# Kernel optimization log

Hardware: AMD Instinct MI355X
Metric: run time of the kernel (lower is better)

The kernel has to match this reference:

```python
import jax, jax.numpy as jnp
import numpy as np
import math

N_BITS = 3
N_EMBD = 2048
N_HEAD = 16
B, T = 1, 2048


def fake_quant_act(x, bits=N_BITS):
    # Brevitas Int8ActPerTensorFloat at 3 bits: signed, non-narrow range [-4, 3]
    qmin, qmax = -(2 ** (bits - 1)), 2 ** (bits - 1) - 1
    s = jax.lax.stop_gradient(jnp.max(jnp.abs(x))) / (2 ** (bits - 1))
    q = jnp.clip(jnp.round(x / s), qmin, qmax) * s
    return x + jax.lax.stop_gradient(q - x)  # STE


def fake_quant_weight(w, bits=N_BITS):
    # Int8WeightPerTensorFloat, narrow_range=True at 3 bits: range [-3, 3]
    qmax = 2 ** (bits - 1) - 1
    s = jax.lax.stop_gradient(jnp.max(jnp.abs(w))) / qmax
    q = jnp.clip(jnp.round(w / s), -qmax, qmax) * s
    return w + jax.lax.stop_gradient(q - w)  # STE


def setup_inputs() -> dict:
    key = jax.random.key(0)
    ks = jax.random.split(key, 7)
    W_STD = 0.02  # GPT-style init keeps exp(att) in range (own_softmax has no max-subtract)
    x = jax.random.normal(ks[0], (B, T, N_EMBD), dtype=jnp.float32)
    W1 = jax.random.normal(ks[1], (N_EMBD, N_EMBD), dtype=jnp.float32) * W_STD
    W2 = jax.random.normal(ks[2], (N_EMBD, N_EMBD), dtype=jnp.float32) * W_STD
    W3 = jax.random.normal(ks[3], (N_EMBD, N_EMBD), dtype=jnp.float32) * W_STD
    b1 = jax.random.normal(ks[4], (N_EMBD,), dtype=jnp.float32) * W_STD
    b2 = jax.random.normal(ks[5], (N_EMBD,), dtype=jnp.float32) * W_STD
    b3 = jax.random.normal(ks[6], (N_EMBD,), dtype=jnp.float32) * W_STD
    return {"x": x, "W1": W1, "b1": b1, "W2": W2, "b2": b2, "W3": W3, "b3": b3}


def reference(x, W1, b1, W2, b2, W3, b3):
    hs = N_EMBD // N_HEAD
    xq = fake_quant_act(x)  # quant_inp
    q = xq @ fake_quant_weight(W1).T + b1  # c_attn1
    k = xq @ fake_quant_weight(W2).T + b2  # c_attn2
    v = xq @ fake_quant_weight(W3).T + b3  # c_attn3
    # [B,T,C] -> [B,nh,T,hs]
    q = q.reshape(B, T, N_HEAD, hs).transpose(0, 2, 1, 3)
    k = k.reshape(B, T, N_HEAD, hs).transpose(0, 2, 1, 3)
    v = v.reshape(B, T, N_HEAD, hs).transpose(0, 2, 1, 3)
    att = jnp.einsum("bhqd,bhkd->bhqk", q, k) * (1.0 / math.sqrt(hs))
    # own_softmax: exp normalized over dim=1 == the HEAD axis (faithful to source; no mask)
    e = jnp.exp(att)
    att = e / jnp.sum(e, axis=1, keepdims=True)
    # attn_dropout p=0 -> identity; c_proj never applied in forward
    y = jnp.einsum("bhqk,bhkd->bhqd", att, v)  # [B,nh,T,hs]
    return y
```

## Files before the change

### kernel.cpp

```cpp
#include <hip/hip_runtime.h>
#include <hip/hip_bf16.h>

typedef short bf16x8 __attribute__((ext_vector_type(8)));
typedef float f32x4 __attribute__((ext_vector_type(4)));
typedef unsigned short u16;

constexpr int TOKS = 2048;
constexpr int EMB  = 2048;
constexpr int NH   = 16;
constexpr int HS   = 128;
constexpr float RSQ = 0.08838834764831845f;

constexpr size_t OFF_SCAL = 0;
constexpr size_t OFF_QX   = 1024;
constexpr size_t SZ_MAT   = (size_t)TOKS * EMB * 2;
constexpr size_t OFF_QW   = OFF_QX + SZ_MAT;
constexpr size_t OFF_Q    = OFF_QW + 3 * SZ_MAT;
constexpr size_t OFF_K    = OFF_Q + SZ_MAT;
constexpr size_t OFF_V    = OFF_K + SZ_MAT;
constexpr size_t OFF_VT   = OFF_V + SZ_MAT;
constexpr size_t OFF_DEN  = OFF_VT + SZ_MAT;

#define VMCNT(n) asm volatile("s_waitcnt vmcnt(" #n ")" ::: "memory")
#define LGKM0()  asm volatile("s_waitcnt lgkmcnt(0)" ::: "memory")
#define BAR()    do { asm volatile("" ::: "memory"); __builtin_amdgcn_s_barrier(); asm volatile("" ::: "memory"); } while (0)

__device__ __forceinline__ u16 f2b(float f) {
  unsigned u = __float_as_uint(f);
  unsigned r = (u + 0x7fffu + ((u >> 16) & 1u)) >> 16;
  return (u16)r;
}

__device__ __forceinline__ unsigned cvtpk(float a, float b) {
  unsigned r;
  asm("v_cvt_pk_bf16_f32 %0, %1, %2" : "=v"(r) : "v"(a), "v"(b));
  return r;
}

__device__ __forceinline__ void gload16(const void* g, void* l) {
  __builtin_amdgcn_global_load_lds(
      (const __attribute__((address_space(1))) unsigned int*)g,
      (__attribute__((address_space(3))) unsigned int*)l, 16, 0, 0);
}

__global__ void k_init(int* scal) {
  if (threadIdx.x < 4) scal[threadIdx.x] = 0;
}

__global__ void k_absmax(const float* __restrict__ x, const float* __restrict__ w1,
                         const float* __restrict__ w2, const float* __restrict__ w3,
                         int* scal) {
  const float* src = (blockIdx.y == 0) ? x : (blockIdx.y == 1) ? w1 : (blockIdx.y == 2) ? w2 : w3;
  const float4* s4 = (const float4*)src;
  int idx = blockIdx.x * 256 + threadIdx.x;
  float m = 0.f;
  for (int i = 0; i < 16; ++i) {
    float4 v = s4[idx + i * 65536];
    m = fmaxf(m, fmaxf(fmaxf(fabsf(v.x), fabsf(v.y)), fmaxf(fabsf(v.z), fabsf(v.w))));
  }
  for (int o = 32; o; o >>= 1) m = fmaxf(m, __shfl_down(m, o));
  __shared__ float red[4];
  if ((threadIdx.x & 63) == 0) red[threadIdx.x >> 6] = m;
  __syncthreads();
  if (threadIdx.x == 0) {
    m = fmaxf(fmaxf(red[0], red[1]), fmaxf(red[2], red[3]));
    atomicMax(&scal[blockIdx.y], __float_as_int(m));
  }
}

__global__ void k_quant(const float* __restrict__ x, const float* __restrict__ w1,
                        const float* __restrict__ w2, const float* __restrict__ w3,
                        u16* qx, u16* qw, const int* scal) {
  int a = blockIdx.y;
  const float* src = (a == 0) ? x : (a == 1) ? w1 : (a == 2) ? w2 : w3;
  u16* dst = (a == 0) ? qx : qw + (size_t)(a - 1) * TOKS * EMB;
  float mx = __int_as_float(scal[a]);
  float s = (a == 0) ? mx * 0.25f : mx / 3.0f;
  float lo = (a == 0) ? -4.f : -3.f;
  const float hi = 3.f;
  int idx = blockIdx.x * 256 + threadIdx.x;
  for (int i = 0; i < 16; ++i) {
    int j = idx + i * 65536;
    float4 v = ((const float4*)src)[j];
    ushort4 o;
    o.x = f2b(fminf(fmaxf(rintf(v.x / s), lo), hi));
    o.y = f2b(fminf(fmaxf(rintf(v.y / s), lo), hi));
    o.z = f2b(fminf(fmaxf(rintf(v.z / s), lo), hi));
    o.w = f2b(fminf(fmaxf(rintf(v.w / s), lo), hi));
    ((ushort4*)dst)[j] = o;
  }
}

__global__ __launch_bounds__(256, 3) void k_gemm(const u16* __restrict__ qx, const u16* __restrict__ qw,
    const float* __restrict__ b1, const float* __restrict__ b2, const float* __restrict__ b3,
    const int* __restrict__ scal, u16* qo, u16* ko, u16* vo) {
  int z = blockIdx.z;
  const u16* W = qw + (size_t)z * TOKS * EMB;
  const float* bias = (z == 0) ? b1 : (z == 1) ? b2 : b3;
  u16* out = (z == 0) ? qo : (z == 1) ? ko : vo;
  float sx = __int_as_float(scal[0]) * 0.25f;
  float sw = __int_as_float(scal[1 + z]) / 3.0f;
  float alpha = sx * sw;
  float extra = (z == 0) ? RSQ : 1.0f;
  int t0 = blockIdx.y * 128, o0 = blockIdx.x * 128;
  __shared__ __align__(16) u16 As[128 * 64];
  __shared__ __align__(16) u16 Bs[128 * 64];
  int tid = threadIdx.x, lane = tid & 63, wid = tid >> 6;
  int mh = (wid >> 1) * 64, nh = (wid & 1) * 64;
  f32x4 acc[4][4] = {};
  const char* Ab = (const char*)qx;
  const char* Bb = (const char*)W;
  for (int kk = 0; kk < 32; ++kk) {
#pragma unroll
    for (int p = 0; p < 4; ++p) {
      int L = p * 4096 + tid * 16;
      int r = L >> 7;
      int s = ((L >> 4) & 7) ^ (r & 7);
      gload16(Ab + (size_t)(t0 + r) * 4096 + kk * 128 + s * 16,
              (char*)As + p * 4096 + wid * 1024);
      gload16(Bb + (size_t)(o0 + r) * 4096 + kk * 128 + s * 16,
              (char*)Bs + p * 4096 + wid * 1024);
    }
    __syncthreads();
#pragma unroll
    for (int ks = 0; ks < 2; ++ks) {
      bf16x8 af[4], bfr[4];
#pragma unroll
      for (int m = 0; m < 4; ++m) {
        int row = mh + m * 16 + (lane & 15);
        int sl = (ks * 4 + (lane >> 4)) ^ (row & 7);
        af[m] = *(const bf16x8*)((const char*)As + row * 128 + sl * 16);
      }
#pragma unroll
      for (int n = 0; n < 4; ++n) {
        int row = nh + n * 16 + (lane & 15);
        int sl = (ks * 4 + (lane >> 4)) ^ (row & 7);
        bfr[n] = *(const bf16x8*)((const char*)Bs + row * 128 + sl * 16);
      }
#pragma unroll
      for (int m = 0; m < 4; ++m)
#pragma unroll
        for (int n = 0; n < 4; ++n)
          acc[m][n] = __builtin_amdgcn_mfma_f32_16x16x32_bf16(af[m], bfr[n], acc[m][n], 0, 0, 0);
    }
    __syncthreads();
  }
#pragma unroll
  for (int m = 0; m < 4; ++m)
#pragma unroll
    for (int n = 0; n < 4; ++n) {
      int ocol = o0 + nh + n * 16 + (lane & 15);
      float bb = bias[ocol];
#pragma unroll
      for (int r = 0; r < 4; ++r) {
        int trow = t0 + mh + m * 16 + (lane >> 4) * 4 + r;
        float v = (acc[m][n][r] * alpha + bb) * extra;
        out[(size_t)trow * EMB + ocol] = f2b(v);
      }
    }
}

__global__ void k_transpose(const u16* __restrict__ v, u16* vt) {
  int h = blockIdx.z, d0 = blockIdx.y * 64, t0 = blockIdx.x * 64;
  __shared__ u16 tile[64][65];
  int tid = threadIdx.x;
  for (int i = 0; i < 16; ++i) {
    int idx = i * 256 + tid, r = idx >> 6, c = idx & 63;
    tile[r][c] = v[(size_t)(t0 + r) * EMB + h * HS + d0 + c];
  }
  __syncthreads();
  for (int i = 0; i < 16; ++i) {
    int idx = i * 256 + tid, r = idx >> 6, c = idx & 63;
    vt[(size_t)(h * HS + d0 + r) * TOKS + t0 + c] = tile[c][r];
  }
}

__global__ __launch_bounds__(256, 3) void k_denom(const u16* __restrict__ q, const u16* __restrict__ k,
                                                  float* __restrict__ invden) {
  int bid = blockIdx.x;
  int qy = bid & 15, kx = bid >> 4;
  int qt0 = qy * 128, kt0 = kx * 64;
  __shared__ __align__(16) u16 Qs[2][128 * 64];
  __shared__ __align__(16) u16 Ksm[2][64 * 64];
  int tid = threadIdx.x, lane = tid & 63, wid = tid >> 6;
  int wq = (wid >> 1) * 64, wk = (wid & 1) * 32;
  f32x4 acc[4][2] = {}, dd[4][2] = {};
  auto stage = [&](int st, int buf) {
#pragma unroll
    for (int p = 0; p < 4; ++p) {
      int L = p * 4096 + tid * 16;
      int r = L >> 7;
      int s = ((L >> 4) & 7) ^ (r & 7);
      gload16((const char*)q + (size_t)(qt0 + r) * 4096 + st * 128 + s * 16,
              (char*)Qs[buf] + p * 4096 + wid * 1024);
    }
#pragma unroll
    for (int p = 0; p < 2; ++p) {
      int L = p * 4096 + tid * 16;
      int r = L >> 7;
      int s = ((L >> 4) & 7) ^ (r & 7);
      gload16((const char*)k + (size_t)(kt0 + r) * 4096 + st * 128 + s * 16,
              (char*)Ksm[buf] + p * 4096 + wid * 1024);
    }
  };
  stage(0, 0);
  for (int st = 0; st < 32; ++st) {
    int cur = st & 1;
    if (st < 31) { stage(st + 1, cur ^ 1); VMCNT(6); } else { VMCNT(0); }
    BAR();
    __builtin_amdgcn_s_setprio(1);
#pragma unroll
    for (int ks = 0; ks < 2; ++ks) {
      bf16x8 af[4], bfr[2];
#pragma unroll
      for (int m = 0; m < 4; ++m) {
        int row = wq + m * 16 + (lane & 15);
        int sl = (ks * 4 + (lane >> 4)) ^ (row & 7);
        af[m] = *(const bf16x8*)((const char*)Qs[cur] + row * 128 + sl * 16);
      }
#pragma unroll
      for (int n = 0; n < 2; ++n) {
        int row = wk + n * 16 + (lane & 15);
        int sl = (ks * 4 + (lane >> 4)) ^ (row & 7);
        bfr[n] = *(const bf16x8*)((const char*)Ksm[cur] + row * 128 + sl * 16);
      }
#pragma unroll
      for (int m = 0; m < 4; ++m)
#pragma unroll
        for (int n = 0; n < 2; ++n)
          acc[m][n] = __builtin_amdgcn_mfma_f32_16x16x32_bf16(af[m], bfr[n], acc[m][n], 0, 0, 0);
    }
    __builtin_amdgcn_s_setprio(0);
    BAR();
    if (st & 1) {
#pragma unroll
      for (int m = 0; m < 4; ++m)
#pragma unroll
        for (int n = 0; n < 2; ++n) {
#pragma unroll
          for (int r = 0; r < 4; ++r) dd[m][n][r] += __expf(acc[m][n][r]);
          acc[m][n] = f32x4{0.f, 0.f, 0.f, 0.f};
        }
    }
  }
#pragma unroll
  for (int m = 0; m < 4; ++m)
#pragma unroll
    for (int n = 0; n < 2; ++n)
#pragma unroll
      for (int r = 0; r < 4; ++r) {
        int qrow = qt0 + wq + m * 16 + (lane >> 4) * 4 + r;
        int kcol = kt0 + wk + n * 16 + (lane & 15);
        invden[(size_t)qrow * TOKS + kcol] = 1.0f / dd[m][n][r];
      }
}

__global__ __launch_bounds__(256, 2) void k_attn(const u16* __restrict__ q, const u16* __restrict__ k,
                                                 const u16* __restrict__ vt, const float* __restrict__ invden,
                                                 float* __restrict__ out) {
  int bid = blockIdx.x;
  int h = bid & 15, qt0 = (bid >> 4) * 64;
  __shared__ __align__(16) u16 Ks[2][64 * 128];
  __shared__ __align__(16) u16 Vs[2][128 * 64];
  __shared__ __align__(16) u16 Ps[64 * 64];
  int tid = threadIdx.x, lane = tid & 63, wid = tid >> 6;

  auto stageKV = [&](int kb, int buf) {
#pragma unroll
    for (int p = 0; p < 4; ++p) {
      int L = p * 4096 + tid * 16;
      int r = L >> 8;
      int s = ((L >> 4) & 15) ^ (r & 7);
      gload16((const char*)k + (size_t)(kb * 64 + r) * 4096 + h * 256 + s * 16,
              (char*)Ks[buf] + p * 4096 + wid * 1024);
    }
#pragma unroll
    for (int p = 0; p < 4; ++p) {
      int L = p * 4096 + tid * 16;
      int r = L >> 7;
      int s = ((L >> 4) & 7) ^ (r & 7);
      gload16((const char*)vt + (size_t)(h * HS + r) * 4096 + kb * 128 + s * 16,
              (char*)Vs[buf] + p * 4096 + wid * 1024);
    }
  };
  stageKV(0, 0);
  bf16x8 qf[4][4];
#pragma unroll
  for (int m = 0; m < 4; ++m)
#pragma unroll
    for (int c = 0; c < 4; ++c)
      qf[m][c] = *(const bf16x8*)(q + (size_t)(qt0 + m * 16 + (lane & 15)) * EMB
                                  + h * HS + c * 32 + (lane >> 4) * 8);
  f32x4 yacc[4][2] = {};
  const float* dinv = invden + (size_t)qt0 * TOKS;
  for (int kb = 0; kb < 32; ++kb) {
    int cur = kb & 1;
    if (kb < 31) { stageKV(kb + 1, cur ^ 1); VMCNT(12); } else { VMCNT(4); }
    BAR();
    f32x4 pacc[4] = {};
    __builtin_amdgcn_s_setprio(1);
#pragma unroll
    for (int c = 0; c < 4; ++c) {
      int row = wid * 16 + (lane & 15);
      int sl = (c * 4 + (lane >> 4)) ^ (row & 7);
      bf16x8 bk = *(const bf16x8*)((const char*)Ks[cur] + row * 256 + sl * 16);
#pragma unroll
      for (int m = 0; m < 4; ++m)
        pacc[m] = __builtin_amdgcn_mfma_f32_16x16x32_bf16(bk, qf[m][c], pacc[m], 0, 0, 0);
    }
    __builtin_amdgcn_s_setprio(0);
#pragma unroll
    for (int m = 0; m < 4; ++m) {
      int qr = m * 16 + (lane & 15);
      float4 dv = *(const float4*)&dinv[(size_t)qr * TOKS + kb * 64 + wid * 16 + (lane >> 4) * 4];
      float e0 = __expf(pacc[m][0]) * dv.x;
      float e1 = __expf(pacc[m][1]) * dv.y;
      float e2 = __expf(pacc[m][2]) * dv.z;
      float e3 = __expf(pacc[m][3]) * dv.w;
      uint2 pk;
      pk.x = cvtpk(e0, e1);
      pk.y = cvtpk(e2, e3);
      int kby = wid * 32 + (lane >> 4) * 8;
      *(uint2*)((char*)Ps + qr * 128 + (kby ^ ((qr & 7) << 4))) = pk;
    }
    if (kb < 31) { VMCNT(8); } else { VMCNT(0); }
    LGKM0();
    BAR();
    __builtin_amdgcn_s_setprio(1);
#pragma unroll
    for (int ks = 0; ks < 2; ++ks) {
      bf16x8 pa[4], bv[2];
#pragma unroll
      for (int m = 0; m < 4; ++m) {
        int row = m * 16 + (lane & 15);
        int off = (ks * 64 + (lane >> 4) * 16) ^ ((row & 7) << 4);
        pa[m] = *(const bf16x8*)((const char*)Ps + row * 128 + off);
      }
#pragma unroll
      for (int j = 0; j < 2; ++j) {
        int row = wid * 32 + j * 16 + (lane & 15);
        int sl = (ks * 4 + (lane >> 4)) ^ (row & 7);
        bv[j] = *(const bf16x8*)((const char*)Vs[cur] + row * 128 + sl * 16);
      }
#pragma unroll
      for (int m = 0; m < 4; ++m)
#pragma unroll
        for (int j = 0; j < 2; ++j)
          yacc[m][j] = __builtin_amdgcn_mfma_f32_16x16x32_bf16(pa[m], bv[j], yacc[m][j], 0, 0, 0);
    }
    __builtin_amdgcn_s_setprio(0);
    BAR();
  }
#pragma unroll
  for (int m = 0; m < 4; ++m)
#pragma unroll
    for (int j = 0; j < 2; ++j)
#pragma unroll
      for (int r = 0; r < 4; ++r) {
        int trow = qt0 + m * 16 + (lane >> 4) * 4 + r;
        int dcol = wid * 32 + j * 16 + (lane & 15);
        out[(size_t)(h * TOKS + trow) * HS + dcol] = yacc[m][j][r];
      }
}

extern "C" void kernel_launch(void* const* d_in, const int* in_sizes, int n_in,
                              void* d_out, int out_size, void* d_ws, size_t ws_size,
                              hipStream_t stream) {
  const float* x  = (const float*)d_in[0];
  const float* W1 = (const float*)d_in[1];
  const float* b1 = (const float*)d_in[2];
  const float* W2 = (const float*)d_in[3];
  const float* b2 = (const float*)d_in[4];
  const float* W3 = (const float*)d_in[5];
  const float* b3 = (const float*)d_in[6];
  char* ws = (char*)d_ws;
  int*   scal   = (int*)(ws + OFF_SCAL);
  u16*   qx     = (u16*)(ws + OFF_QX);
  u16*   qw     = (u16*)(ws + OFF_QW);
  u16*   qo     = (u16*)(ws + OFF_Q);
  u16*   ko     = (u16*)(ws + OFF_K);
  u16*   vo     = (u16*)(ws + OFF_V);
  u16*   vt     = (u16*)(ws + OFF_VT);
  float* invden = (float*)(ws + OFF_DEN);
  float* y      = (float*)d_out;

  hipLaunchKernelGGL(k_init, dim3(1), dim3(64), 0, stream, scal);
  hipLaunchKernelGGL(k_absmax, dim3(256, 4), dim3(256), 0, stream, x, W1, W2, W3, scal);
  hipLaunchKernelGGL(k_quant, dim3(256, 4), dim3(256), 0, stream, x, W1, W2, W3, qx, qw, scal);
  hipLaunchKernelGGL(k_gemm, dim3(16, 16, 3), dim3(256), 0, stream,
                     qx, qw, b1, b2, b3, scal, qo, ko, vo);
  hipLaunchKernelGGL(k_transpose, dim3(32, 2, 16), dim3(256), 0, stream, vo, vt);
  hipLaunchKernelGGL(k_denom, dim3(512), dim3(256), 0, stream, qo, ko, invden);
  hipLaunchKernelGGL(k_attn, dim3(512), dim3(256), 0, stream, qo, ko, vt, invden, y);
}
```

Before: 207.5 us.

## Store inverse denominators as bf16 and prefetch them one block ahead

The inverse softmax denominators go from fp32 to bf16, which halves the 16 MB write in k_denom and the matching read in k_attn. k_attn now prefetches the next key block's denominators into registers alongside the K/V stage, ping-ponging between two register sets in a manually unrolled loop. This removes the blocking global load before the exp step. The head/block mapping is also permuted to change L2 locality. The cost is reduced precision of the denominators and higher register pressure.

```diff
diff --git a/kernel.cpp b/kernel.cpp
--- a/kernel.cpp
+++ b/kernel.cpp
@@ -176,7 +176,7 @@
 }
 
 __global__ __launch_bounds__(256, 3) void k_denom(const u16* __restrict__ q, const u16* __restrict__ k,
-                                                  float* __restrict__ invden) {
+                                                  u16* __restrict__ invden) {
   int bid = blockIdx.x;
   int qy = bid & 15, kx = bid >> 4;
   int qt0 = qy * 128, kt0 = kx * 64;
@@ -251,15 +251,16 @@
       for (int r = 0; r < 4; ++r) {
         int qrow = qt0 + wq + m * 16 + (lane >> 4) * 4 + r;
         int kcol = kt0 + wk + n * 16 + (lane & 15);
-        invden[(size_t)qrow * TOKS + kcol] = 1.0f / dd[m][n][r];
+        invden[(size_t)qrow * TOKS + kcol] = f2b(1.0f / dd[m][n][r]);
       }
 }
 
 __global__ __launch_bounds__(256, 2) void k_attn(const u16* __restrict__ q, const u16* __restrict__ k,
-                                                 const u16* __restrict__ vt, const float* __restrict__ invden,
+                                                 const u16* __restrict__ vt, const u16* __restrict__ invden,
                                                  float* __restrict__ out) {
   int bid = blockIdx.x;
-  int h = bid & 15, qt0 = (bid >> 4) * 64;
+  int h = (bid & 7) * 2 + ((bid >> 3) & 1);
+  int qt0 = (bid >> 4) * 64;
   __shared__ __align__(16) u16 Ks[2][64 * 128];
   __shared__ __align__(16) u16 Vs[2][128 * 64];
   __shared__ __align__(16) u16 Ps[64 * 64];
@@ -283,7 +284,15 @@
               (char*)Vs[buf] + p * 4096 + wid * 1024);
     }
   };
+  const u16* dinv = invden + (size_t)qt0 * TOKS;
+  uint2 dvA[4], dvB[4];
+
   stageKV(0, 0);
+#pragma unroll
+  for (int m = 0; m < 4; ++m) {
+    int qr = m * 16 + (lane & 15);
+    dvA[m] = *(const uint2*)&dinv[(size_t)qr * TOKS + wid * 16 + (lane >> 4) * 4];
+  }
   bf16x8 qf[4][4];
 #pragma unroll
   for (int m = 0; m < 4; ++m)
@@ -292,65 +301,88 @@
       qf[m][c] = *(const bf16x8*)(q + (size_t)(qt0 + m * 16 + (lane & 15)) * EMB
                                   + h * HS + c * 32 + (lane >> 4) * 8);
   f32x4 yacc[4][2] = {};
-  const float* dinv = invden + (size_t)qt0 * TOKS;
-  for (int kb = 0; kb < 32; ++kb) {
-    int cur = kb & 1;
-    if (kb < 31) { stageKV(kb + 1, cur ^ 1); VMCNT(12); } else { VMCNT(4); }
-    BAR();
-    f32x4 pacc[4] = {};
-    __builtin_amdgcn_s_setprio(1);
-#pragma unroll
-    for (int c = 0; c < 4; ++c) {
-      int row = wid * 16 + (lane & 15);
-      int sl = (c * 4 + (lane >> 4)) ^ (row & 7);
-      bf16x8 bk = *(const bf16x8*)((const char*)Ks[cur] + row * 256 + sl * 16);
-#pragma unroll
-      for (int m = 0; m < 4; ++m)
-        pacc[m] = __builtin_amdgcn_mfma_f32_16x16x32_bf16(bk, qf[m][c], pacc[m], 0, 0, 0);
-    }
-    __builtin_amdgcn_s_setprio(0);
-#pragma unroll
-    for (int m = 0; m < 4; ++m) {
-      int qr = m * 16 + (lane & 15);
-      float4 dv = *(const float4*)&dinv[(size_t)qr * TOKS + kb * 64 + wid * 16 + (lane >> 4) * 4];
-      float e0 = __expf(pacc[m][0]) * dv.x;
-      float e1 = __expf(pacc[m][1]) * dv.y;
-      float e2 = __expf(pacc[m][2]) * dv.z;
-      float e3 = __expf(pacc[m][3]) * dv.w;
-      uint2 pk;
-      pk.x = cvtpk(e0, e1);
-      pk.y = cvtpk(e2, e3);
-      int kby = wid * 32 + (lane >> 4) * 8;
-      *(uint2*)((char*)Ps + qr * 128 + (kby ^ ((qr & 7) << 4))) = pk;
-    }
-    if (kb < 31) { VMCNT(8); } else { VMCNT(0); }
-    LGKM0();
-    BAR();
-    __builtin_amdgcn_s_setprio(1);
-#pragma unroll
-    for (int ks = 0; ks < 2; ++ks) {
-      bf16x8 pa[4], bv[2];
-#pragma unroll
-      for (int m = 0; m < 4; ++m) {
-        int row = m * 16 + (lane & 15);
-        int off = (ks * 64 + (lane >> 4) * 16) ^ ((row & 7) << 4);
-        pa[m] = *(const bf16x8*)((const char*)Ps + row * 128 + off);
-      }
-#pragma unroll
-      for (int j = 0; j < 2; ++j) {
-        int row = wid * 32 + j * 16 + (lane & 15);
-        int sl = (ks * 4 + (lane >> 4)) ^ (row & 7);
-        bv[j] = *(const bf16x8*)((const char*)Vs[cur] + row * 128 + sl * 16);
-      }
-#pragma unroll
-      for (int m = 0; m < 4; ++m)
-#pragma unroll
-        for (int j = 0; j < 2; ++j)
-          yacc[m][j] = __builtin_amdgcn_mfma_f32_16x16x32_bf16(pa[m], bv[j], yacc[m][j], 0, 0, 0);
-    }
-    __builtin_amdgcn_s_setprio(0);
-    BAR();
-  }
+
+#define ITER(KB, CUR, DVU, DVP, LAST)                                           \
+  {                                                                             \
+    if (!(LAST)) {                                                              \
+      stageKV((KB) + 1, (CUR) ^ 1);                                             \
+      _Pragma("unroll")                                                         \
+      for (int m = 0; m < 4; ++m) {                                             \
+        int qr = m * 16 + (lane & 15);                                          \
+        DVP[m] = *(const uint2*)&dinv[(size_t)qr * TOKS + ((KB) + 1) * 64 +     \
+                                      wid * 16 + (lane >> 4) * 4];              \
+      }                                                                         \
+      VMCNT(12);                                                                \
+    } else {                                                                    \
+      VMCNT(0);                                                                 \
+    }                                                                           \
+    BAR();                                                                      \
+    f32x4 pacc[4] = {};                                                         \
+    __builtin_amdgcn_s_setprio(1);                                              \
+    _Pragma("unroll")                                                           \
+    for (int c = 0; c < 4; ++c) {                                               \
+      int row = wid * 16 + (lane & 15);                                         \
+      int sl = (c * 4 + (lane >> 4)) ^ (row & 7);                               \
+      bf16x8 bk = *(const bf16x8*)((const char*)Ks[CUR] + row * 256 + sl * 16); \
+      _Pragma("unroll")                                                         \
+      for (int m = 0; m < 4; ++m)                                               \
+        pacc[m] = __builtin_amdgcn_mfma_f32_16x16x32_bf16(bk, qf[m][c], pacc[m], 0, 0, 0); \
+    }                                                                           \
+    __builtin_amdgcn_s_setprio(0);                                              \
+    _Pragma("unroll")                                                           \
+    for (int m = 0; m < 4; ++m) {                                               \
+      int qr = m * 16 + (lane & 15);                                            \
+      float d0 = __uint_as_float(DVU[m].x << 16);                               \
+      float d1 = __uint_as_float(DVU[m].x & 0xffff0000u);                       \
+      float d2 = __uint_as_float(DVU[m].y << 16);                               \
+      float d3 = __uint_as_float(DVU[m].y & 0xffff0000u);                       \
+      float e0 = __expf(pacc[m][0]) * d0;                                       \
+      float e1 = __expf(pacc[m][1]) * d1;                                       \
+      float e2 = __expf(pacc[m][2]) * d2;                                       \
+      float e3 = __expf(pacc[m][3]) * d3;                                       \
+      uint2 pk;                                                                 \
+      pk.x = cvtpk(e0, e1);                                                     \
+      pk.y = cvtpk(e2, e3);                                                     \
+      int kby = wid * 32 + (lane >> 4) * 8;                                     \
+      *(uint2*)((char*)Ps + qr * 128 + (kby ^ ((qr & 7) << 4))) = pk;           \
+    }                                                                           \
+    LGKM0();                                                                    \
+    BAR();                                                                      \
+    __builtin_amdgcn_s_setprio(1);                                              \
+    _Pragma("unroll")                                                           \
+    for (int ks = 0; ks < 2; ++ks) {                                            \
+      bf16x8 pa[4], bv[2];                                                      \
+      _Pragma("unroll")                                                         \
+      for (int m = 0; m < 4; ++m) {                                             \
+        int row = m * 16 + (lane & 15);                                         \
+        int off = (ks * 64 + (lane >> 4) * 16) ^ ((row & 7) << 4);              \
+        pa[m] = *(const bf16x8*)((const char*)Ps + row * 128 + off);            \
+      }                                                                         \
+      _Pragma("unroll")                                                         \
+      for (int j = 0; j < 2; ++j) {                                             \
+        int row = wid * 32 + j * 16 + (lane & 15);                              \
+        int sl = (ks * 4 + (lane >> 4)) ^ (row & 7);                            \
+        bv[j] = *(const bf16x8*)((const char*)Vs[CUR] + row * 128 + sl * 16);   \
+      }                                                                         \
+      _Pragma("unroll")                                                         \
+      for (int m = 0; m < 4; ++m)                                               \
+        _Pragma("unroll")                                                       \
+        for (int j = 0; j < 2; ++j)                                             \
+          yacc[m][j] = __builtin_amdgcn_mfma_f32_16x16x32_bf16(pa[m], bv[j], yacc[m][j], 0, 0, 0); \
+    }                                                                           \
+    __builtin_amdgcn_s_setprio(0);                                              \
+    BAR();                                                                      \
+  }
+
+  for (int t = 0; t < 15; ++t) {
+    int kbE = 2 * t, kbO = 2 * t + 1;
+    ITER(kbE, 0, dvA, dvB, false);
+    ITER(kbO, 1, dvB, dvA, false);
+  }
+  ITER(30, 0, dvA, dvB, false);
+  ITER(31, 1, dvB, dvA, true);
+#undef ITER
+
 #pragma unroll
   for (int m = 0; m < 4; ++m)
 #pragma unroll
@@ -381,7 +413,7 @@
   u16*   ko     = (u16*)(ws + OFF_K);
   u16*   vo     = (u16*)(ws + OFF_V);
   u16*   vt     = (u16*)(ws + OFF_VT);
-  float* invden = (float*)(ws + OFF_DEN);
+  u16*   invden = (u16*)(ws + OFF_DEN);
   float* y      = (float*)d_out;
 
   hipLaunchKernelGGL(k_init, dim3(1), dim3(64), 0, stream, scal);
```

Result: faster. 193.3 us (-6.8%).
